# Kernel tuning notes

Hardware: AMD Instinct MI355X
Metric: run time of the kernel (lower is better)

## Reference

```python
import jax, jax.numpy as jnp
import numpy as np

D_MODEL = 1024
NUM_HEADS = 16
DEPTH = D_MODEL // NUM_HEADS


def setup_inputs() -> dict:
    key = jax.random.key(0)
    k_x, k_q, k_k, k_v, k_f = jax.random.split(key, 5)
    scale = 1.0 / np.sqrt(D_MODEL)
    return {
        "x": jax.random.normal(k_x, (4, 2048, D_MODEL), dtype=jnp.float32),
        "wq": jax.random.normal(k_q, (D_MODEL, D_MODEL), dtype=jnp.float32) * scale,
        "wk": jax.random.normal(k_k, (D_MODEL, D_MODEL), dtype=jnp.float32) * scale,
        "wv": jax.random.normal(k_v, (D_MODEL, D_MODEL), dtype=jnp.float32) * scale,
        "wf": jax.random.normal(k_f, (D_MODEL, D_MODEL), dtype=jnp.float32) * scale,
    }


def reference(x, wq, wk, wv, wf):
    B, S, _ = x.shape
    # nn.Linear(y) = y @ W.T; weights stored [out, in]
    def proj(w):
        y = jnp.einsum('bsd,ed->bse', x, w)
        return y.reshape(B, S, NUM_HEADS, DEPTH).transpose(0, 2, 1, 3)  # [B,H,S,depth]
    q, k, v = proj(wq), proj(wk), proj(wv)
    scores = jnp.einsum('bhqd,bhkd->bhqk', q, k) / jnp.sqrt(jnp.float32(DEPTH))
    attn = jax.nn.softmax(scores, axis=-1)
    out = jnp.einsum('bhqk,bhkd->bhqd', attn, v)
    out = out.transpose(0, 2, 1, 3).reshape(B, S, D_MODEL)
    return jnp.einsum('bsd,ed->bse', out, wf)
```

## Files before the change

kernel.cpp:

```cpp
#include <hip/hip_runtime.h>

typedef unsigned short u16;
typedef unsigned int u32;
typedef __attribute__((ext_vector_type(8))) short bvec8;
typedef __attribute__((ext_vector_type(4))) float fvec4;
typedef __attribute__((ext_vector_type(2))) u32 uvec2;

__device__ __forceinline__ u16 f2bf(float f) {
  unsigned int b = __float_as_uint(f);
  b += 0x7FFFu + ((b >> 16) & 1u);
  return (u16)(b >> 16);
}

__device__ __forceinline__ u32 pk_bf16(float a, float b) {
  u32 t0 = __float_as_uint(a) + 0x8000u;
  u32 t1 = __float_as_uint(b) + 0x8000u;
  return __builtin_amdgcn_perm(t1, t0, 0x07060302u);
}

__device__ __forceinline__ void gl_lds16(const void* g, void* l) {
  __builtin_amdgcn_global_load_lds(
      (__attribute__((address_space(1))) const unsigned int*)g,
      (__attribute__((address_space(3))) unsigned int*)l, 16, 0, 0);
}

__global__ __launch_bounds__(256) void cvt_all(
    const float* __restrict__ x,  const float* __restrict__ wq,
    const float* __restrict__ wk, const float* __restrict__ wv,
    const float* __restrict__ wf,
    u16* __restrict__ xb, u16* __restrict__ wqb, u16* __restrict__ wkb,
    u16* __restrict__ wvb, u16* __restrict__ wfb) {
  int b = blockIdx.x;
  const float* in; u16* out; int base;
  if (b < 8192) { in = x; out = xb; base = b; }
  else {
    int t = (b - 8192) >> 10, rb = (b - 8192) & 1023;
    in  = t == 0 ? wq  : t == 1 ? wk  : t == 2 ? wv  : wf;
    out = t == 0 ? wqb : t == 1 ? wkb : t == 2 ? wvb : wfb;
    base = rb;
  }
  int i = base * 256 + threadIdx.x;
  float4 v = ((const float4*)in)[i];
  ushort4 o;
  o.x = f2bf(v.x); o.y = f2bf(v.y); o.z = f2bf(v.z); o.w = f2bf(v.w);
  ((ushort4*)out)[i] = o;
}

struct GemmCore {
  fvec4 acc[4][4];
  int wm, wn, lanelo, quad;
  __device__ __forceinline__ void run(const u16* __restrict__ A,
                                      const u16* __restrict__ W,
                                      u16* As, u16* Bs,
                                      int m0, int n0, int tid) {
    const int w = tid >> 6, lane = tid & 63;
    lanelo = lane & 15; quad = lane >> 4;
    wm = (w & 1) * 64; wn = (w >> 1) * 64;
#pragma unroll
    for (int i = 0; i < 4; ++i)
#pragma unroll
      for (int j = 0; j < 4; ++j) acc[i][j] = fvec4{0.f, 0.f, 0.f, 0.f};

    const int s = (lanelo ^ (lanelo >> 2)) & 3;
    const int abase = (wm + lanelo) * 32 + ((quad ^ s) << 3);
    const int bbase = (wn + lanelo) * 32 + ((quad ^ s) << 3);

    const u16* gA[2]; const u16* gB[2]; int ldso[2];
#pragma unroll
    for (int t = 0; t < 2; ++t) {
      int idx = (w * 2 + t) * 64 + lane;
      int row = idx >> 2, bs = idx & 3;
      int sw = (row ^ (row >> 2)) & 3;
      gA[t] = A + (m0 + row) * 1024 + ((bs ^ sw) << 3);
      gB[t] = W + (n0 + row) * 1024 + ((bs ^ sw) << 3);
      ldso[t] = (w * 2 + t) * 512;
    }

    for (int k0 = 0; k0 < 1024; k0 += 32) {
      __syncthreads();
#pragma unroll
      for (int t = 0; t < 2; ++t) {
        gl_lds16(gA[t] + k0, &As[ldso[t]]);
        gl_lds16(gB[t] + k0, &Bs[ldso[t]]);
      }
      __syncthreads();
      bvec8 a[4], b[4];
#pragma unroll
      for (int i = 0; i < 4; ++i) a[i] = *(const bvec8*)&As[abase + i * 512];
#pragma unroll
      for (int j = 0; j < 4; ++j) b[j] = *(const bvec8*)&Bs[bbase + j * 512];
#pragma unroll
      for (int i = 0; i < 4; ++i)
#pragma unroll
        for (int j = 0; j < 4; ++j)
          acc[i][j] = __builtin_amdgcn_mfma_f32_16x16x32_bf16(a[i], b[j], acc[i][j], 0, 0, 0);
    }
  }
};

__global__ __launch_bounds__(256, 3) void gemm_qkv(
    const u16* __restrict__ A, const u16* __restrict__ Wq,
    const u16* __restrict__ Wk, const u16* __restrict__ Wv,
    u16* __restrict__ Qb, u16* __restrict__ Kb, u16* __restrict__ Vt) {
  __shared__ u16 As[128 * 32];
  __shared__ u16 Bs[128 * 32];
  const int z = blockIdx.z;
  const u16* W = z == 0 ? Wq : z == 1 ? Wk : Wv;
  const int m0 = blockIdx.x * 128, n0 = blockIdx.y * 128;
  GemmCore g;
  g.run(A, W, As, Bs, m0, n0, threadIdx.x);

  if (z == 2) {
#pragma unroll
    for (int i = 0; i < 4; ++i) {
      const int mg = m0 + g.wm + i * 16 + g.quad * 4;
      const int bidx = mg >> 11, srow = mg & 2047;
#pragma unroll
      for (int j = 0; j < 4; ++j) {
        const int ng = n0 + g.wn + j * 16 + g.lanelo;
        const int hh = ng >> 6, dd = ng & 63;
        ushort4 pk;
        pk.x = f2bf(g.acc[i][j][0]); pk.y = f2bf(g.acc[i][j][1]);
        pk.z = f2bf(g.acc[i][j][2]); pk.w = f2bf(g.acc[i][j][3]);
        *(ushort4*)&Vt[(bidx * 16 + hh) * 131072 + dd * 2048 + srow] = pk;
      }
    }
  } else {
    const float scale = (z == 0) ? 0.18033688011112042f : 1.0f;
    u16* C = (z == 0) ? Qb : Kb;
#pragma unroll
    for (int i = 0; i < 4; ++i) {
      const int mg0 = m0 + g.wm + i * 16 + g.quad * 4;
#pragma unroll
      for (int j = 0; j < 4; ++j) {
        const int ng = n0 + g.wn + j * 16 + g.lanelo;
        const int hh = ng >> 6, dd = ng & 63;
#pragma unroll
        for (int r = 0; r < 4; ++r) {
          const int mg = mg0 + r;
          C[((mg >> 11) * 16 + hh) * 131072 + (mg & 2047) * 64 + dd] =
              f2bf(g.acc[i][j][r] * scale);
        }
      }
    }
  }
}

__global__ __launch_bounds__(256, 2) void gemm_final(const u16* __restrict__ A,
                                                     const u16* __restrict__ W,
                                                     float* __restrict__ C) {
  __shared__ u16 As[128 * 32];
  __shared__ u16 Bs[128 * 32];
  const int m0 = blockIdx.x * 128, n0 = blockIdx.y * 128;
  GemmCore g;
  g.run(A, W, As, Bs, m0, n0, threadIdx.x);
#pragma unroll
  for (int i = 0; i < 4; ++i) {
    const int mg = m0 + g.wm + i * 16 + g.quad * 4;
#pragma unroll
    for (int j = 0; j < 4; ++j) {
      const int ng = n0 + g.wn + j * 16 + g.lanelo;
#pragma unroll
      for (int r = 0; r < 4; ++r) C[(mg + r) * 1024 + ng] = g.acc[i][j][r];
    }
  }
}

__global__ __launch_bounds__(512, 4) void attn(const u16* __restrict__ Qb,
                                               const u16* __restrict__ Kb,
                                               const u16* __restrict__ Vt,
                                               u16* __restrict__ Ob) {
  __shared__ u16 Ks[128 * 64];
  __shared__ u16 Vs[64 * 128];
  __shared__ u16 Ps[8][32 * 64];
  const int tid = threadIdx.x;
  const int w = tid >> 6, lane = tid & 63;
  const int lanelo = lane & 15, quad = lane >> 4;
  const int bh = blockIdx.x;
  const int sq0 = blockIdx.y * 256 + w * 32;
  const u16* Qh = Qb + bh * 131072;
  const u16* Kh = Kb + bh * 131072;
  const u16* Vh = Vt + bh * 131072;
  u16* Pw = Ps[w];

  bvec8 aq[2][2];
#pragma unroll
  for (int qb = 0; qb < 2; ++qb)
#pragma unroll
    for (int kk = 0; kk < 2; ++kk)
      aq[qb][kk] = *(const bvec8*)&Qh[(sq0 + qb * 16 + lanelo) * 64 + kk * 32 + quad * 8];

  bvec8 ones;
#pragma unroll
  for (int j = 0; j < 8; ++j) ones[j] = (short)0x3F80;

  fvec4 o[2][4] = {};
  fvec4 lacc[2] = {};

  const u16* gK[2]; const u16* gV[2]; int ldof[2];
#pragma unroll
  for (int t = 0; t < 2; ++t) {
    int idx = (w * 2 + t) * 64 + lane;
    int rk = idx >> 3, bk = idx & 7;
    gK[t] = Kh + rk * 64 + ((bk ^ (rk & 7)) << 3);
    int rv = idx >> 4, bv = idx & 15;
    gV[t] = Vh + rv * 2048 + ((bv ^ (rv & 15)) << 3);
    ldof[t] = (w * 2 + t) * 512;
  }
  int kfb[2];
#pragma unroll
  for (int kk = 0; kk < 2; ++kk)
    kfb[kk] = lanelo * 64 + (((kk * 4 + quad) ^ (lanelo & 7)) << 3);
  int vfb[4];
#pragma unroll
  for (int c = 0; c < 4; ++c)
    vfb[c] = lanelo * 128 + (((c * 4 + quad) ^ lanelo) << 3);
  const int pwb = lanelo * 64 + (quad & 1) * 4;
  const int pxr = lanelo & 7;
  const int pqh = quad >> 1;

  for (int sk0 = 0; sk0 < 2048; sk0 += 128) {
    __syncthreads();
#pragma unroll
    for (int t = 0; t < 2; ++t) {
      gl_lds16(gK[t] + sk0 * 64, &Ks[ldof[t]]);
      gl_lds16(gV[t] + sk0, &Vs[ldof[t]]);
    }
    __syncthreads();

#pragma unroll
    for (int h = 0; h < 2; ++h) {
      fvec4 sa[2][4] = {};
#pragma unroll
      for (int jb = 0; jb < 4; ++jb) {
#pragma unroll
        for (int kk = 0; kk < 2; ++kk) {
          bvec8 kf = *(const bvec8*)&Ks[(h * 4 + jb) * 1024 + kfb[kk]];
          sa[0][jb] = __builtin_amdgcn_mfma_f32_16x16x32_bf16(kf, aq[0][kk], sa[0][jb], 0, 0, 0);
          sa[1][jb] = __builtin_amdgcn_mfma_f32_16x16x32_bf16(kf, aq[1][kk], sa[1][jb], 0, 0, 0);
        }
      }

#pragma unroll
      for (int qb = 0; qb < 2; ++qb) {
#pragma unroll
        for (int jb = 0; jb < 4; ++jb) {
          float p0 = __builtin_amdgcn_exp2f(sa[qb][jb][0]);
          float p1 = __builtin_amdgcn_exp2f(sa[qb][jb][1]);
          float p2 = __builtin_amdgcn_exp2f(sa[qb][jb][2]);
          float p3 = __builtin_amdgcn_exp2f(sa[qb][jb][3]);
          uvec2 pk;
          pk.x = pk_bf16(p0, p1);
          pk.y = pk_bf16(p2, p3);
          *(uvec2*)&Pw[qb * 1024 + pwb + (((jb * 2 + pqh) ^ pxr) << 3)] = pk;
        }
      }

#pragma unroll
      for (int cc = 0; cc < 2; ++cc) {
        bvec8 ap0 = *(const bvec8*)&Pw[kfb[cc]];
        bvec8 ap1 = *(const bvec8*)&Pw[1024 + kfb[cc]];
        lacc[0] = __builtin_amdgcn_mfma_f32_16x16x32_bf16(ap0, ones, lacc[0], 0, 0, 0);
        lacc[1] = __builtin_amdgcn_mfma_f32_16x16x32_bf16(ap1, ones, lacc[1], 0, 0, 0);
        const int c = h * 2 + cc;
#pragma unroll
        for (int dj = 0; dj < 4; ++dj) {
          bvec8 bv = *(const bvec8*)&Vs[dj * 2048 + vfb[c]];
          o[0][dj] = __builtin_amdgcn_mfma_f32_16x16x32_bf16(ap0, bv, o[0][dj], 0, 0, 0);
          o[1][dj] = __builtin_amdgcn_mfma_f32_16x16x32_bf16(ap1, bv, o[1][dj], 0, 0, 0);
        }
      }
    }
  }

  const int b = bh >> 4, hh = bh & 15;
#pragma unroll
  for (int qb = 0; qb < 2; ++qb) {
#pragma unroll
    for (int r = 0; r < 4; ++r) {
      const float inv = 1.0f / lacc[qb][r];
      const int sg = sq0 + qb * 16 + quad * 4 + r;
#pragma unroll
      for (int dj = 0; dj < 4; ++dj)
        Ob[((b * 2048 + sg) * 16 + hh) * 64 + dj * 16 + lanelo] = f2bf(o[qb][dj][r] * inv);
    }
  }
}

extern "C" void kernel_launch(void* const* d_in, const int* in_sizes, int n_in,
                              void* d_out, int out_size, void* d_ws, size_t ws_size,
                              hipStream_t stream) {
  (void)in_sizes; (void)n_in; (void)out_size; (void)ws_size;
  const float* x  = (const float*)d_in[0];
  const float* wq = (const float*)d_in[1];
  const float* wk = (const float*)d_in[2];
  const float* wv = (const float*)d_in[3];
  const float* wf = (const float*)d_in[4];

  char* ws = (char*)d_ws;
  u16* xb  = (u16*)ws;
  u16* wqb = (u16*)(ws + 16777216);
  u16* wkb = (u16*)(ws + 18874368);
  u16* wvb = (u16*)(ws + 20971520);
  u16* wfb = (u16*)(ws + 23068672);
  u16* Qb  = (u16*)(ws + 25165824);
  u16* Kb  = (u16*)(ws + 41943040);
  u16* Vt  = (u16*)(ws + 58720256);
  u16* Ob  = xb;

  cvt_all<<<12288, 256, 0, stream>>>(x, wq, wk, wv, wf, xb, wqb, wkb, wvb, wfb);
  gemm_qkv<<<dim3(64, 8, 3), 256, 0, stream>>>(xb, wqb, wkb, wvb, Qb, Kb, Vt);
  attn<<<dim3(64, 8), 512, 0, stream>>>(Qb, Kb, Vt, Ob);
  gemm_final<<<dim3(64, 8), 256, 0, stream>>>(Ob, wfb, (float*)d_out);
}
```

Measured before the change: 260.3 us.

## Transpose MFMA operands for vectorized epilogue stores and widen attention query tiles

The GEMM core is templated to swap the MFMA A/B operands, so each lane holds four consecutive output columns. This lets the Q/K and final-projection epilogues write ushort4 and float4 vectors instead of scalar strided stores, and the V projection moves to its own launch that keeps the old layout. Attention now uses 256-thread blocks where each wave handles 64 query rows instead of 32. That doubles reuse of each K/V fragment read from LDS and halves the number of waves sharing the loads, and the P scratch layout changes to a padded stride instead of an XOR swizzle. The costs are more register pressure in attention, fewer waves per block to hide latency, and an extra kernel launch.

```diff
diff --git a/kernel.cpp b/kernel.cpp
--- a/kernel.cpp
+++ b/kernel.cpp
@@ -46,6 +46,7 @@
   ((ushort4*)out)[i] = o;
 }
 
+template<bool TR>
 struct GemmCore {
   fvec4 acc[4][4];
   int wm, wn, lanelo, quad;
@@ -93,55 +94,59 @@
       for (int i = 0; i < 4; ++i)
 #pragma unroll
         for (int j = 0; j < 4; ++j)
-          acc[i][j] = __builtin_amdgcn_mfma_f32_16x16x32_bf16(a[i], b[j], acc[i][j], 0, 0, 0);
+          acc[i][j] = TR
+            ? __builtin_amdgcn_mfma_f32_16x16x32_bf16(b[j], a[i], acc[i][j], 0, 0, 0)
+            : __builtin_amdgcn_mfma_f32_16x16x32_bf16(a[i], b[j], acc[i][j], 0, 0, 0);
     }
   }
 };
 
-__global__ __launch_bounds__(256, 3) void gemm_qkv(
+__global__ __launch_bounds__(256, 3) void gemm_qk(
     const u16* __restrict__ A, const u16* __restrict__ Wq,
-    const u16* __restrict__ Wk, const u16* __restrict__ Wv,
-    u16* __restrict__ Qb, u16* __restrict__ Kb, u16* __restrict__ Vt) {
+    const u16* __restrict__ Wk, u16* __restrict__ Qb, u16* __restrict__ Kb) {
   __shared__ u16 As[128 * 32];
   __shared__ u16 Bs[128 * 32];
   const int z = blockIdx.z;
-  const u16* W = z == 0 ? Wq : z == 1 ? Wk : Wv;
   const int m0 = blockIdx.x * 128, n0 = blockIdx.y * 128;
-  GemmCore g;
-  g.run(A, W, As, Bs, m0, n0, threadIdx.x);
-
-  if (z == 2) {
-#pragma unroll
-    for (int i = 0; i < 4; ++i) {
-      const int mg = m0 + g.wm + i * 16 + g.quad * 4;
-      const int bidx = mg >> 11, srow = mg & 2047;
-#pragma unroll
-      for (int j = 0; j < 4; ++j) {
-        const int ng = n0 + g.wn + j * 16 + g.lanelo;
-        const int hh = ng >> 6, dd = ng & 63;
-        ushort4 pk;
-        pk.x = f2bf(g.acc[i][j][0]); pk.y = f2bf(g.acc[i][j][1]);
-        pk.z = f2bf(g.acc[i][j][2]); pk.w = f2bf(g.acc[i][j][3]);
-        *(ushort4*)&Vt[(bidx * 16 + hh) * 131072 + dd * 2048 + srow] = pk;
-      }
-    }
-  } else {
-    const float scale = (z == 0) ? 0.18033688011112042f : 1.0f;
-    u16* C = (z == 0) ? Qb : Kb;
-#pragma unroll
-    for (int i = 0; i < 4; ++i) {
-      const int mg0 = m0 + g.wm + i * 16 + g.quad * 4;
-#pragma unroll
-      for (int j = 0; j < 4; ++j) {
-        const int ng = n0 + g.wn + j * 16 + g.lanelo;
-        const int hh = ng >> 6, dd = ng & 63;
-#pragma unroll
-        for (int r = 0; r < 4; ++r) {
-          const int mg = mg0 + r;
-          C[((mg >> 11) * 16 + hh) * 131072 + (mg & 2047) * 64 + dd] =
-              f2bf(g.acc[i][j][r] * scale);
-        }
-      }
+  GemmCore<true> g;
+  g.run(A, z == 0 ? Wq : Wk, As, Bs, m0, n0, threadIdx.x);
+  const float scale = (z == 0) ? 0.18033688011112042f : 1.0f;
+  u16* C = (z == 0) ? Qb : Kb;
+#pragma unroll
+  for (int i = 0; i < 4; ++i) {
+    const int sg = m0 + g.wm + i * 16 + g.lanelo;
+    const int srow = sg & 2047, bidx = sg >> 11;
+#pragma unroll
+    for (int j = 0; j < 4; ++j) {
+      const int e0 = n0 + g.wn + j * 16 + g.quad * 4;
+      const int hh = e0 >> 6, dd = e0 & 63;
+      ushort4 pk;
+      pk.x = f2bf(g.acc[i][j][0] * scale); pk.y = f2bf(g.acc[i][j][1] * scale);
+      pk.z = f2bf(g.acc[i][j][2] * scale); pk.w = f2bf(g.acc[i][j][3] * scale);
+      *(ushort4*)&C[(bidx * 16 + hh) * 131072 + srow * 64 + dd] = pk;
+    }
+  }
+}
+
+__global__ __launch_bounds__(256, 3) void gemm_v(
+    const u16* __restrict__ A, const u16* __restrict__ Wv, u16* __restrict__ Vt) {
+  __shared__ u16 As[128 * 32];
+  __shared__ u16 Bs[128 * 32];
+  const int m0 = blockIdx.x * 128, n0 = blockIdx.y * 128;
+  GemmCore<false> g;
+  g.run(A, Wv, As, Bs, m0, n0, threadIdx.x);
+#pragma unroll
+  for (int i = 0; i < 4; ++i) {
+    const int mg = m0 + g.wm + i * 16 + g.quad * 4;
+    const int bidx = mg >> 11, srow = mg & 2047;
+#pragma unroll
+    for (int j = 0; j < 4; ++j) {
+      const int ng = n0 + g.wn + j * 16 + g.lanelo;
+      const int hh = ng >> 6, dd = ng & 63;
+      ushort4 pk;
+      pk.x = f2bf(g.acc[i][j][0]); pk.y = f2bf(g.acc[i][j][1]);
+      pk.z = f2bf(g.acc[i][j][2]); pk.w = f2bf(g.acc[i][j][3]);
+      *(ushort4*)&Vt[(bidx * 16 + hh) * 131072 + dd * 2048 + srow] = pk;
     }
   }
 }
@@ -152,40 +157,41 @@
   __shared__ u16 As[128 * 32];
   __shared__ u16 Bs[128 * 32];
   const int m0 = blockIdx.x * 128, n0 = blockIdx.y * 128;
-  GemmCore g;
+  GemmCore<true> g;
   g.run(A, W, As, Bs, m0, n0, threadIdx.x);
 #pragma unroll
   for (int i = 0; i < 4; ++i) {
-    const int mg = m0 + g.wm + i * 16 + g.quad * 4;
+    const int sg = m0 + g.wm + i * 16 + g.lanelo;
 #pragma unroll
     for (int j = 0; j < 4; ++j) {
-      const int ng = n0 + g.wn + j * 16 + g.lanelo;
-#pragma unroll
-      for (int r = 0; r < 4; ++r) C[(mg + r) * 1024 + ng] = g.acc[i][j][r];
-    }
-  }
-}
-
-__global__ __launch_bounds__(512, 4) void attn(const u16* __restrict__ Qb,
+      const int e0 = n0 + g.wn + j * 16 + g.quad * 4;
+      float4 v = {g.acc[i][j][0], g.acc[i][j][1], g.acc[i][j][2], g.acc[i][j][3]};
+      *(float4*)&C[sg * 1024 + e0] = v;
+    }
+  }
+}
+
+#define PSTRIDE 40
+__global__ __launch_bounds__(256, 3) void attn(const u16* __restrict__ Qb,
                                                const u16* __restrict__ Kb,
                                                const u16* __restrict__ Vt,
                                                u16* __restrict__ Ob) {
   __shared__ u16 Ks[128 * 64];
   __shared__ u16 Vs[64 * 128];
-  __shared__ u16 Ps[8][32 * 64];
+  __shared__ u16 Ps[4][64 * PSTRIDE];
   const int tid = threadIdx.x;
   const int w = tid >> 6, lane = tid & 63;
   const int lanelo = lane & 15, quad = lane >> 4;
   const int bh = blockIdx.x;
-  const int sq0 = blockIdx.y * 256 + w * 32;
+  const int sq0 = blockIdx.y * 256 + w * 64;
   const u16* Qh = Qb + bh * 131072;
   const u16* Kh = Kb + bh * 131072;
   const u16* Vh = Vt + bh * 131072;
   u16* Pw = Ps[w];
 
-  bvec8 aq[2][2];
-#pragma unroll
-  for (int qb = 0; qb < 2; ++qb)
+  bvec8 aq[4][2];
+#pragma unroll
+  for (int qb = 0; qb < 4; ++qb)
 #pragma unroll
     for (int kk = 0; kk < 2; ++kk)
       aq[qb][kk] = *(const bvec8*)&Qh[(sq0 + qb * 16 + lanelo) * 64 + kk * 32 + quad * 8];
@@ -194,18 +200,18 @@
 #pragma unroll
   for (int j = 0; j < 8; ++j) ones[j] = (short)0x3F80;
 
-  fvec4 o[2][4] = {};
-  fvec4 lacc[2] = {};
-
-  const u16* gK[2]; const u16* gV[2]; int ldof[2];
-#pragma unroll
-  for (int t = 0; t < 2; ++t) {
-    int idx = (w * 2 + t) * 64 + lane;
+  fvec4 o[4][4] = {};
+  fvec4 lacc[4] = {};
+
+  const u16* gK[4]; const u16* gV[4]; int ldof[4];
+#pragma unroll
+  for (int t = 0; t < 4; ++t) {
+    int idx = (w * 4 + t) * 64 + lane;
     int rk = idx >> 3, bk = idx & 7;
     gK[t] = Kh + rk * 64 + ((bk ^ (rk & 7)) << 3);
     int rv = idx >> 4, bv = idx & 15;
     gV[t] = Vh + rv * 2048 + ((bv ^ (rv & 15)) << 3);
-    ldof[t] = (w * 2 + t) * 512;
+    ldof[t] = (w * 4 + t) * 512;
   }
   int kfb[2];
 #pragma unroll
@@ -215,36 +221,36 @@
 #pragma unroll
   for (int c = 0; c < 4; ++c)
     vfb[c] = lanelo * 128 + (((c * 4 + quad) ^ lanelo) << 3);
-  const int pwb = lanelo * 64 + (quad & 1) * 4;
-  const int pxr = lanelo & 7;
-  const int pqh = quad >> 1;
+  const int pwb = lanelo * PSTRIDE + quad * 4;
+  const int prb = lanelo * PSTRIDE + quad * 8;
 
   for (int sk0 = 0; sk0 < 2048; sk0 += 128) {
     __syncthreads();
 #pragma unroll
-    for (int t = 0; t < 2; ++t) {
+    for (int t = 0; t < 4; ++t) {
       gl_lds16(gK[t] + sk0 * 64, &Ks[ldof[t]]);
       gl_lds16(gV[t] + sk0, &Vs[ldof[t]]);
     }
     __syncthreads();
 
 #pragma unroll
-    for (int h = 0; h < 2; ++h) {
-      fvec4 sa[2][4] = {};
-#pragma unroll
-      for (int jb = 0; jb < 4; ++jb) {
+    for (int qq = 0; qq < 4; ++qq) {
+      fvec4 sa[4][2] = {};
+#pragma unroll
+      for (int jb = 0; jb < 2; ++jb) {
 #pragma unroll
         for (int kk = 0; kk < 2; ++kk) {
-          bvec8 kf = *(const bvec8*)&Ks[(h * 4 + jb) * 1024 + kfb[kk]];
-          sa[0][jb] = __builtin_amdgcn_mfma_f32_16x16x32_bf16(kf, aq[0][kk], sa[0][jb], 0, 0, 0);
-          sa[1][jb] = __builtin_amdgcn_mfma_f32_16x16x32_bf16(kf, aq[1][kk], sa[1][jb], 0, 0, 0);
+          bvec8 kf = *(const bvec8*)&Ks[(qq * 2 + jb) * 1024 + kfb[kk]];
+#pragma unroll
+          for (int qb = 0; qb < 4; ++qb)
+            sa[qb][jb] = __builtin_amdgcn_mfma_f32_16x16x32_bf16(kf, aq[qb][kk], sa[qb][jb], 0, 0, 0);
         }
       }
 
 #pragma unroll
-      for (int qb = 0; qb < 2; ++qb) {
-#pragma unroll
-        for (int jb = 0; jb < 4; ++jb) {
+      for (int qb = 0; qb < 4; ++qb) {
+#pragma unroll
+        for (int jb = 0; jb < 2; ++jb) {
           float p0 = __builtin_amdgcn_exp2f(sa[qb][jb][0]);
           float p1 = __builtin_amdgcn_exp2f(sa[qb][jb][1]);
           float p2 = __builtin_amdgcn_exp2f(sa[qb][jb][2]);
@@ -252,22 +258,18 @@
           uvec2 pk;
           pk.x = pk_bf16(p0, p1);
           pk.y = pk_bf16(p2, p3);
-          *(uvec2*)&Pw[qb * 1024 + pwb + (((jb * 2 + pqh) ^ pxr) << 3)] = pk;
+          *(uvec2*)&Pw[qb * 16 * PSTRIDE + pwb + jb * 16] = pk;
         }
       }
 
 #pragma unroll
-      for (int cc = 0; cc < 2; ++cc) {
-        bvec8 ap0 = *(const bvec8*)&Pw[kfb[cc]];
-        bvec8 ap1 = *(const bvec8*)&Pw[1024 + kfb[cc]];
-        lacc[0] = __builtin_amdgcn_mfma_f32_16x16x32_bf16(ap0, ones, lacc[0], 0, 0, 0);
-        lacc[1] = __builtin_amdgcn_mfma_f32_16x16x32_bf16(ap1, ones, lacc[1], 0, 0, 0);
-        const int c = h * 2 + cc;
+      for (int qb = 0; qb < 4; ++qb) {
+        bvec8 ap = *(const bvec8*)&Pw[qb * 16 * PSTRIDE + prb];
+        lacc[qb] = __builtin_amdgcn_mfma_f32_16x16x32_bf16(ap, ones, lacc[qb], 0, 0, 0);
 #pragma unroll
         for (int dj = 0; dj < 4; ++dj) {
-          bvec8 bv = *(const bvec8*)&Vs[dj * 2048 + vfb[c]];
-          o[0][dj] = __builtin_amdgcn_mfma_f32_16x16x32_bf16(ap0, bv, o[0][dj], 0, 0, 0);
-          o[1][dj] = __builtin_amdgcn_mfma_f32_16x16x32_bf16(ap1, bv, o[1][dj], 0, 0, 0);
+          bvec8 bv = *(const bvec8*)&Vs[dj * 2048 + vfb[qq]];
+          o[qb][dj] = __builtin_amdgcn_mfma_f32_16x16x32_bf16(ap, bv, o[qb][dj], 0, 0, 0);
         }
       }
     }
@@ -275,7 +277,7 @@
 
   const int b = bh >> 4, hh = bh & 15;
 #pragma unroll
-  for (int qb = 0; qb < 2; ++qb) {
+  for (int qb = 0; qb < 4; ++qb) {
 #pragma unroll
     for (int r = 0; r < 4; ++r) {
       const float inv = 1.0f / lacc[qb][r];
@@ -309,7 +311,8 @@
   u16* Ob  = xb;
 
   cvt_all<<<12288, 256, 0, stream>>>(x, wq, wk, wv, wf, xb, wqb, wkb, wvb, wfb);
-  gemm_qkv<<<dim3(64, 8, 3), 256, 0, stream>>>(xb, wqb, wkb, wvb, Qb, Kb, Vt);
-  attn<<<dim3(64, 8), 512, 0, stream>>>(Qb, Kb, Vt, Ob);
+  gemm_qk<<<dim3(64, 8, 2), 256, 0, stream>>>(xb, wqb, wkb, Qb, Kb);
+  gemm_v<<<dim3(64, 8), 256, 0, stream>>>(xb, wvb, Vt);
+  attn<<<dim3(64, 8), 256, 0, stream>>>(Qb, Kb, Vt, Ob);
   gemm_final<<<dim3(64, 8), 256, 0, stream>>>(Ob, wfb, (float*)d_out);
 }
```

After: 347.8 us. 33.6% more time.
